# Kernel tuning notes

Measured on AMD Instinct MI355X. Metric: run time of the kernel, lower is better.

Reference implementation:

```python
import jax, jax.numpy as jnp
import numpy as np

D_MODEL = 1024
NUM_HEADS = 16
D_K = D_MODEL // NUM_HEADS


def setup_inputs() -> dict:
    key = jax.random.key(0)
    ks = jax.random.split(key, 7)
    B, S = 4, 2048
    lim = float(np.sqrt(6.0 / (D_MODEL + D_MODEL)))  # xavier uniform
    x = jax.random.normal(ks[0], (B, S, D_MODEL), dtype=jnp.float32)
    w_q = jax.random.uniform(ks[1], (D_MODEL, D_MODEL), jnp.float32, -lim, lim)
    w_k = jax.random.uniform(ks[2], (D_MODEL, D_MODEL), jnp.float32, -lim, lim)
    w_v = jax.random.uniform(ks[3], (D_MODEL, D_MODEL), jnp.float32, -lim, lim)
    w_o = jax.random.uniform(ks[4], (D_MODEL, D_MODEL), jnp.float32, -lim, lim)
    b_o = jnp.zeros((D_MODEL,), jnp.float32)
    ln_g = jnp.ones((D_MODEL,), jnp.float32)
    ln_b = jnp.zeros((D_MODEL,), jnp.float32)
    return {"x": x, "w_q": w_q, "w_k": w_k, "w_v": w_v, "w_o": w_o,
            "b_o": b_o, "ln_g": ln_g, "ln_b": ln_b}


def _layer_norm(y, g, b, eps=1e-5):
    mu = jnp.mean(y, axis=-1, keepdims=True)
    var = jnp.var(y, axis=-1, keepdims=True)
    return (y - mu) * jax.lax.rsqrt(var + eps) * g + b


def reference(x, w_q, w_k, w_v, w_o, b_o, ln_g, ln_b):
    B, S, D = x.shape
    # Linear weights stored torch-style [out, in]: y = x @ W^T
    def proj(w):
        return jnp.einsum('bsd,ed->bse', x, w).reshape(B, S, NUM_HEADS, D_K).transpose(0, 2, 1, 3)
    Q, K, V = proj(w_q), proj(w_k), proj(w_v)  # [B, H, S, d_k]
    scores = jnp.einsum('bhqd,bhkd->bhqk', Q, K) / jnp.sqrt(jnp.float32(D_K))
    attn = jax.nn.softmax(scores, axis=-1)  # dropout identity at eval
    out = jnp.einsum('bhqk,bhkd->bhqd', attn, V)  # [B, H, S, d_k]
    out = out.transpose(0, 2, 1, 3).reshape(B, S, D)
    out = jnp.einsum('bsd,ed->bse', out, w_o) + b_o
    return _layer_norm(x + out, ln_g, ln_b)
```

## Files before the change

### kernel.cpp

```cpp
#include <hip/hip_runtime.h>

typedef __bf16 bf16;
typedef bf16 v8bf __attribute__((ext_vector_type(8)));
typedef bf16 v4bf __attribute__((ext_vector_type(4)));
typedef float v4f __attribute__((ext_vector_type(4)));

#define GAS __attribute__((address_space(1)))
#define LAS __attribute__((address_space(3)))

constexpr int D    = 1024;
constexpr int ROWS = 8192;
constexpr int TILE = 128;

__global__ __launch_bounds__(256) void cast_all(
    const float* __restrict__ x,
    const float* __restrict__ wq, const float* __restrict__ wk,
    const float* __restrict__ wv, const float* __restrict__ wo,
    bf16* __restrict__ xb, bf16* __restrict__ wqb, bf16* __restrict__ wkb,
    bf16* __restrict__ wvb, bf16* __restrict__ wob)
{
    int i = blockIdx.x * 256 + threadIdx.x;
    const float* src; bf16* dst; int off;
    if (i < 2 * 1024 * 1024) { src = x; dst = xb; off = i; }
    else {
        int j = i - 2 * 1024 * 1024;
        int w = j >> 18;
        off = j & ((1 << 18) - 1);
        src = (w == 0) ? wq : (w == 1) ? wk : (w == 2) ? wv : wo;
        dst = (w == 0) ? wqb : (w == 1) ? wkb : (w == 2) ? wvb : wob;
    }
    float4 v = ((const float4*)src)[off];
    v4bf o;
    o[0] = (bf16)v.x; o[1] = (bf16)v.y; o[2] = (bf16)v.z; o[3] = (bf16)v.w;
    ((v4bf*)dst)[off] = o;
}

template<int MODE>
__global__ __launch_bounds__(256) void gemm_bt(
    const bf16* __restrict__ A,
    const bf16* __restrict__ W0, const bf16* __restrict__ W1, const bf16* __restrict__ W2,
    bf16* __restrict__ O0, bf16* __restrict__ O1, bf16* __restrict__ O2,
    float* __restrict__ Of, const float* __restrict__ bias,
    const float* __restrict__ X)
{
    __shared__ bf16 As[2][TILE * 32];
    __shared__ bf16 Bs[2][TILE * 32];

    const int tid  = threadIdx.x;
    const int lane = tid & 63;
    const int wave = tid >> 6;
    const int quad = lane >> 4;
    const int l16  = lane & 15;
    const int wm   = (wave >> 1) * 64;
    const int wn   = (wave & 1) * 64;

    const int z = blockIdx.z;
    const bf16* Bw = (MODE == 0) ? ((z == 0) ? W0 : ((z == 1) ? W1 : W2)) : W0;
    bf16*       Ob = (MODE == 0) ? ((z == 0) ? O0 : ((z == 1) ? O1 : O2)) : O0;

    const long rowA0 = (long)blockIdx.y * TILE;
    const long rowB0 = (long)blockIdx.x * TILE;

    const int stRow = wave * 16 + (lane >> 2);
    const int stCol = (lane & 3) * 8;
    const bf16* gA = A  + (rowA0 + stRow) * D + stCol;
    const bf16* gB = Bw + (rowB0 + stRow) * D + stCol;
    const int ldsOff = wave * 16 * 32;

    const v4f vzero = {0.f, 0.f, 0.f, 0.f};
    v4f acc[4][4];
    #pragma unroll
    for (int i = 0; i < 4; i++)
        #pragma unroll
        for (int j = 0; j < 4; j++) acc[i][j] = vzero;

    for (int k0 = 0; k0 < D; k0 += 64) {
        __syncthreads();
        #pragma unroll
        for (int p = 0; p < 2; ++p)
            #pragma unroll
            for (int i = 0; i < 2; ++i) {
                __builtin_amdgcn_global_load_lds(
                    (const GAS void*)(gA + (long)i * 64 * D + p * 32),
                    (LAS void*)(&As[p][ldsOff + i * 64 * 32]), 16, 0, 0);
                __builtin_amdgcn_global_load_lds(
                    (const GAS void*)(gB + (long)i * 64 * D + p * 32),
                    (LAS void*)(&Bs[p][ldsOff + i * 64 * 32]), 16, 0, 0);
            }
        gA += 64; gB += 64;
        __syncthreads();

        #pragma unroll
        for (int p = 0; p < 2; ++p) {
            v8bf a[4], b[4];
            #pragma unroll
            for (int mi = 0; mi < 4; mi++)
                a[mi] = *(const v8bf*)(&As[p][(wm + mi * 16 + l16) * 32 + quad * 8]);
            #pragma unroll
            for (int ni = 0; ni < 4; ni++)
                b[ni] = *(const v8bf*)(&Bs[p][(wn + ni * 16 + l16) * 32 + quad * 8]);
            #pragma unroll
            for (int mi = 0; mi < 4; mi++)
                #pragma unroll
                for (int ni = 0; ni < 4; ni++)
                    acc[mi][ni] = __builtin_amdgcn_mfma_f32_16x16x32_bf16(a[mi], b[ni], acc[mi][ni], 0, 0, 0);
        }
    }

    const float qscale = 0.125f * 1.44269504f;

    if (MODE == 0 && z == 2) {
        #pragma unroll
        for (int mi = 0; mi < 4; mi++) {
            #pragma unroll
            for (int ni = 0; ni < 4; ni++) {
                const long col = rowB0 + wn + ni * 16 + l16;
                const long h_ = col >> 6, dd = col & 63;
                const long row0 = rowA0 + wm + mi * 16 + quad * 4;
                const long b_ = row0 >> 11, s0 = row0 & 2047;
                v4bf pk;
                #pragma unroll
                for (int r = 0; r < 4; r++) pk[r] = (bf16)acc[mi][ni][r];
                *(v4bf*)(Ob + ((b_ * 16 + h_) * 64 + dd) * 2048 + s0) = pk;
            }
        }
    } else {
        #pragma unroll
        for (int mi = 0; mi < 4; mi++) {
            #pragma unroll
            for (int ni = 0; ni < 4; ni++) {
                const long col = rowB0 + wn + ni * 16 + l16;
                float bv = (MODE == 1) ? bias[col] : 0.f;
                #pragma unroll
                for (int r = 0; r < 4; r++) {
                    const long row = rowA0 + wm + mi * 16 + quad * 4 + r;
                    float v = acc[mi][ni][r];
                    if (MODE == 1) Of[row * D + col] = v + bv + X[row * D + col];
                    else {
                        if (z == 0) v *= qscale;
                        Ob[row * D + col] = (bf16)v;
                    }
                }
            }
        }
    }
}

__global__ __launch_bounds__(256) void attn_kernel(
    const bf16* __restrict__ Q, const bf16* __restrict__ Kg,
    const bf16* __restrict__ VtG, bf16* __restrict__ O)
{
    const int qt = blockIdx.x, h = blockIdx.y, b = blockIdx.z;
    const int tid  = threadIdx.x;
    const int lane = tid & 63;
    const int wave = tid >> 6;
    const int quad = lane >> 4;
    const int l16  = lane & 15;

    __shared__ bf16 Kt[64 * 72];
    __shared__ bf16 Vt[64 * 72];
    __shared__ bf16 Ps[4][32 * 72];

    v8bf qB[2][2];
    #pragma unroll
    for (int qf = 0; qf < 2; qf++) {
        const long qrow = (long)(b * 2048 + qt * 128 + wave * 32 + qf * 16 + l16);
        #pragma unroll
        for (int hh = 0; hh < 2; hh++)
            qB[qf][hh] = *(const v8bf*)(Q + qrow * D + h * 64 + hh * 32 + quad * 8);
    }

    float l_acc[2] = {0.f, 0.f};
    v4f o_acc[2][4];
    const v4f vzero = {0.f, 0.f, 0.f, 0.f};
    #pragma unroll
    for (int qf = 0; qf < 2; qf++)
        #pragma unroll
        for (int nf = 0; nf < 4; nf++) o_acc[qf][nf] = vzero;

    const int sC = (tid & 7) * 8;
    const int iR = tid >> 3;

    const bf16* kLane = Kg  + (long)b * 2048 * D + h * 64 + sC + (long)iR * D;
    const bf16* vLane = VtG + (long)(b * 16 + h) * 64 * 2048 + sC + (long)iR * 2048;
    bf16* ktW = Kt + iR * 72 + sC;
    bf16* vtW = Vt + iR * 72 + sC;

    v8bf kpre[2], vpre[2];
    kpre[0] = *(const v8bf*)(kLane);
    kpre[1] = *(const v8bf*)(kLane + 32 * D);
    vpre[0] = *(const v8bf*)(vLane);
    vpre[1] = *(const v8bf*)(vLane + 32 * 2048);
    kLane += 64 * D;
    vLane += 64;

    for (int kt = 0; kt < 32; ++kt) {
        __syncthreads();
        *(v8bf*)(ktW)            = kpre[0];
        *(v8bf*)(ktW + 32 * 72)  = kpre[1];
        *(v8bf*)(vtW)            = vpre[0];
        *(v8bf*)(vtW + 32 * 72)  = vpre[1];
        __syncthreads();

        if (kt + 1 < 32) {
            kpre[0] = *(const v8bf*)(kLane);
            kpre[1] = *(const v8bf*)(kLane + 32 * D);
            vpre[0] = *(const v8bf*)(vLane);
            vpre[1] = *(const v8bf*)(vLane + 32 * 2048);
            kLane += 64 * D;
            vLane += 64;
        }

        v4f st[4][2];
        #pragma unroll
        for (int kf = 0; kf < 4; kf++) {
            v8bf kA0 = *(const v8bf*)(Kt + (kf * 16 + l16) * 72 + quad * 8);
            v8bf kA1 = *(const v8bf*)(Kt + (kf * 16 + l16) * 72 + 32 + quad * 8);
            #pragma unroll
            for (int qf = 0; qf < 2; qf++) {
                v4f t = vzero;
                t = __builtin_amdgcn_mfma_f32_16x16x32_bf16(kA0, qB[qf][0], t, 0, 0, 0);
                t = __builtin_amdgcn_mfma_f32_16x16x32_bf16(kA1, qB[qf][1], t, 0, 0, 0);
                st[kf][qf] = t;
            }
        }

        #pragma unroll
        for (int qf = 0; qf < 2; qf++)
            #pragma unroll
            for (int kf = 0; kf < 4; kf++) {
                v4bf pk;
                #pragma unroll
                for (int r = 0; r < 4; r++) {
                    float p = __builtin_amdgcn_exp2f(st[kf][qf][r]);
                    l_acc[qf] += p;
                    pk[r] = (bf16)p;
                }
                *(v4bf*)(&Ps[wave][(qf * 16 + l16) * 72 + kf * 16 + quad * 4]) = pk;
            }

        #pragma unroll
        for (int ks = 0; ks < 2; ++ks) {
            v8bf vb[4];
            #pragma unroll
            for (int nf = 0; nf < 4; nf++)
                vb[nf] = *(const v8bf*)(Vt + (nf * 16 + l16) * 72 + ks * 32 + quad * 8);
            #pragma unroll
            for (int qf = 0; qf < 2; qf++) {
                v8bf pa = *(const v8bf*)(&Ps[wave][(qf * 16 + l16) * 72 + ks * 32 + quad * 8]);
                #pragma unroll
                for (int nf = 0; nf < 4; nf++)
                    o_acc[qf][nf] = __builtin_amdgcn_mfma_f32_16x16x32_bf16(pa, vb[nf], o_acc[qf][nf], 0, 0, 0);
            }
        }
    }

    #pragma unroll
    for (int qf = 0; qf < 2; qf++) {
        float l = l_acc[qf];
        l += __shfl_xor(l, 16);
        l += __shfl_xor(l, 32);
        l_acc[qf] = l;
    }

    #pragma unroll
    for (int qf = 0; qf < 2; qf++) {
        float inv[4];
        #pragma unroll
        for (int r = 0; r < 4; r++) {
            const int src = (quad << 4) | (quad * 4 + r);
            inv[r] = 1.f / __shfl(l_acc[qf], src);
        }
        const long orow = (long)(b * 2048 + qt * 128 + wave * 32 + qf * 16 + quad * 4);
        #pragma unroll
        for (int nf = 0; nf < 4; nf++)
            #pragma unroll
            for (int r = 0; r < 4; r++)
                O[(orow + r) * D + h * 64 + nf * 16 + l16] = (bf16)(o_acc[qf][nf][r] * inv[r]);
    }
}

__global__ __launch_bounds__(256) void ln_kernel(
    const float* __restrict__ g, const float* __restrict__ beta,
    float* __restrict__ out)
{
    const int row = blockIdx.x;
    const int t = threadIdx.x;
    const int lane = t & 63, wave = t >> 6;
    const long base = (long)row * D + t * 4;

    float4 yv = *(const float4*)(out + base);
    float y0 = yv.x, y1 = yv.y, y2 = yv.z, y3 = yv.w;
    float s1 = y0 + y1 + y2 + y3;
    float s2 = y0*y0 + y1*y1 + y2*y2 + y3*y3;
    #pragma unroll
    for (int off = 1; off < 64; off <<= 1) {
        s1 += __shfl_xor(s1, off);
        s2 += __shfl_xor(s2, off);
    }
    __shared__ float r1[4], r2[4];
    if (lane == 0) { r1[wave] = s1; r2[wave] = s2; }
    __syncthreads();
    float S1 = r1[0] + r1[1] + r1[2] + r1[3];
    float S2 = r2[0] + r2[1] + r2[2] + r2[3];
    float mu  = S1 * (1.f / 1024.f);
    float var = S2 * (1.f / 1024.f) - mu * mu;
    float rsd = rsqrtf(var + 1e-5f);

    float4 gv = *(const float4*)(g + t * 4);
    float4 bv = *(const float4*)(beta + t * 4);
    float4 o;
    o.x = (y0 - mu) * rsd * gv.x + bv.x;
    o.y = (y1 - mu) * rsd * gv.y + bv.y;
    o.z = (y2 - mu) * rsd * gv.z + bv.z;
    o.w = (y3 - mu) * rsd * gv.w + bv.w;
    *(float4*)(out + base) = o;
}

extern "C" void kernel_launch(void* const* d_in, const int* in_sizes, int n_in,
                              void* d_out, int out_size, void* d_ws, size_t ws_size,
                              hipStream_t stream)
{
    const float* x   = (const float*)d_in[0];
    const float* wq  = (const float*)d_in[1];
    const float* wk  = (const float*)d_in[2];
    const float* wv  = (const float*)d_in[3];
    const float* wo  = (const float*)d_in[4];
    const float* bo  = (const float*)d_in[5];
    const float* lng = (const float*)d_in[6];
    const float* lnb = (const float*)d_in[7];
    float* out = (float*)d_out;

    char* ws = (char*)d_ws;
    bf16* xb  = (bf16*)(ws);
    bf16* wqb = (bf16*)(ws + (size_t)16 * 1024 * 1024);
    bf16* wkb = wqb + 1024 * 1024;
    bf16* wvb = wkb + 1024 * 1024;
    bf16* wob = wvb + 1024 * 1024;
    bf16* Qb  = (bf16*)(ws + (size_t)24 * 1024 * 1024);
    bf16* Kb  = Qb + (size_t)ROWS * D;
    bf16* VtG = Kb + (size_t)ROWS * D;
    bf16* Ab  = VtG + (size_t)ROWS * D;

    cast_all<<<12288, 256, 0, stream>>>(x, wq, wk, wv, wo,
                                        xb, wqb, wkb, wvb, wob);

    dim3 gqkv(D / TILE, ROWS / TILE, 3);
    gemm_bt<0><<<gqkv, 256, 0, stream>>>(xb, wqb, wkb, wvb, Qb, Kb, VtG,
                                         nullptr, nullptr, nullptr);

    attn_kernel<<<dim3(16, 16, 4), 256, 0, stream>>>(Qb, Kb, VtG, Ab);

    dim3 gout(D / TILE, ROWS / TILE, 1);
    gemm_bt<1><<<gout, 256, 0, stream>>>(Ab, wob, nullptr, nullptr,
                                         nullptr, nullptr, nullptr, out, bo, x);

    ln_kernel<<<8192, 256, 0, stream>>>(lng, lnb, out);
}
```

Before: 316.6 us.

## Rewrite attention inner loop with 32x32 MFMA and in-register P transpose

Switches the attention kernel from 16x16x32 MFMA tiles to 32x32x16 tiles. The softmax probabilities are converted to bf16 and rearranged across lanes with permlane32 swaps, so they feed the PV MFMA straight from registers instead of going through a per-wave shared-memory buffer. The K/V shared tiles drop their padding and use an XOR swizzle to avoid bank conflicts. The intent is to cut LDS traffic and synchronisation per tile and raise MFMA efficiency, at the cost of inline asm that depends on the exact lane layout.

```diff
diff --git a/kernel.cpp b/kernel.cpp
--- a/kernel.cpp
+++ b/kernel.cpp
@@ -4,6 +4,9 @@
 typedef bf16 v8bf __attribute__((ext_vector_type(8)));
 typedef bf16 v4bf __attribute__((ext_vector_type(4)));
 typedef float v4f __attribute__((ext_vector_type(4)));
+typedef float v16f __attribute__((ext_vector_type(16)));
+typedef unsigned int u32;
+typedef u32 v4u __attribute__((ext_vector_type(4)));
 
 #define GAS __attribute__((address_space(1)))
 #define LAS __attribute__((address_space(3)))
@@ -154,37 +157,33 @@
     const int tid  = threadIdx.x;
     const int lane = tid & 63;
     const int wave = tid >> 6;
-    const int quad = lane >> 4;
-    const int l16  = lane & 15;
-
-    __shared__ bf16 Kt[64 * 72];
-    __shared__ bf16 Vt[64 * 72];
-    __shared__ bf16 Ps[4][32 * 72];
-
-    v8bf qB[2][2];
-    #pragma unroll
-    for (int qf = 0; qf < 2; qf++) {
-        const long qrow = (long)(b * 2048 + qt * 128 + wave * 32 + qf * 16 + l16);
-        #pragma unroll
-        for (int hh = 0; hh < 2; hh++)
-            qB[qf][hh] = *(const v8bf*)(Q + qrow * D + h * 64 + hh * 32 + quad * 8);
-    }
-
-    float l_acc[2] = {0.f, 0.f};
-    v4f o_acc[2][4];
-    const v4f vzero = {0.f, 0.f, 0.f, 0.f};
-    #pragma unroll
-    for (int qf = 0; qf < 2; qf++)
-        #pragma unroll
-        for (int nf = 0; nf < 4; nf++) o_acc[qf][nf] = vzero;
-
-    const int sC = (tid & 7) * 8;
+    const int l31  = lane & 31;
+    const int hi   = lane >> 5;
+
+    __shared__ bf16 Kt[64 * 64];
+    __shared__ bf16 Vt[64 * 64];
+
+    const long qrow = (long)(b * 2048 + qt * 128 + wave * 32 + l31);
+    v8bf qB[4];
+    #pragma unroll
+    for (int f = 0; f < 4; f++)
+        qB[f] = *(const v8bf*)(Q + qrow * D + h * 64 + f * 16 + hi * 8);
+
+    v16f o_acc[2];
+    #pragma unroll
+    for (int d2 = 0; d2 < 2; d2++)
+        #pragma unroll
+        for (int i = 0; i < 16; i++) o_acc[d2][i] = 0.f;
+    float l_acc = 0.f;
+
     const int iR = tid >> 3;
-
+    const int c8 = tid & 7;
+    const int sC = c8 * 8;
     const bf16* kLane = Kg  + (long)b * 2048 * D + h * 64 + sC + (long)iR * D;
     const bf16* vLane = VtG + (long)(b * 16 + h) * 64 * 2048 + sC + (long)iR * 2048;
-    bf16* ktW = Kt + iR * 72 + sC;
-    bf16* vtW = Vt + iR * 72 + sC;
+    const int wOff = iR * 64 + ((c8 ^ (iR & 7)) * 8);
+    bf16* ktW = Kt + wOff;
+    bf16* vtW = Vt + wOff;
 
     v8bf kpre[2], vpre[2];
     kpre[0] = *(const v8bf*)(kLane);
@@ -197,9 +196,9 @@
     for (int kt = 0; kt < 32; ++kt) {
         __syncthreads();
         *(v8bf*)(ktW)            = kpre[0];
-        *(v8bf*)(ktW + 32 * 72)  = kpre[1];
+        *(v8bf*)(ktW + 32 * 64)  = kpre[1];
         *(v8bf*)(vtW)            = vpre[0];
-        *(v8bf*)(vtW + 32 * 72)  = vpre[1];
+        *(v8bf*)(vtW + 32 * 64)  = vpre[1];
         __syncthreads();
 
         if (kt + 1 < 32) {
@@ -211,72 +210,57 @@
             vLane += 64;
         }
 
-        v4f st[4][2];
-        #pragma unroll
-        for (int kf = 0; kf < 4; kf++) {
-            v8bf kA0 = *(const v8bf*)(Kt + (kf * 16 + l16) * 72 + quad * 8);
-            v8bf kA1 = *(const v8bf*)(Kt + (kf * 16 + l16) * 72 + 32 + quad * 8);
-            #pragma unroll
-            for (int qf = 0; qf < 2; qf++) {
-                v4f t = vzero;
-                t = __builtin_amdgcn_mfma_f32_16x16x32_bf16(kA0, qB[qf][0], t, 0, 0, 0);
-                t = __builtin_amdgcn_mfma_f32_16x16x32_bf16(kA1, qB[qf][1], t, 0, 0, 0);
-                st[kf][qf] = t;
-            }
-        }
-
-        #pragma unroll
-        for (int qf = 0; qf < 2; qf++)
-            #pragma unroll
-            for (int kf = 0; kf < 4; kf++) {
-                v4bf pk;
+        #pragma unroll
+        for (int ko = 0; ko < 2; ko++) {
+            v16f st;
+            #pragma unroll
+            for (int i = 0; i < 16; i++) st[i] = 0.f;
+            const int krow = ko * 32 + l31;
+            const int ksw  = krow & 7;
+            #pragma unroll
+            for (int f = 0; f < 4; f++) {
+                v8bf kA = *(const v8bf*)(Kt + krow * 64 + (((2 * f + hi) ^ ksw) * 8));
+                st = __builtin_amdgcn_mfma_f32_32x32x16_bf16(kA, qB[f], st, 0, 0, 0);
+            }
+
+            float p[16];
+            #pragma unroll
+            for (int r = 0; r < 16; r++) {
+                p[r] = __builtin_amdgcn_exp2f(st[r]);
+                l_acc += p[r];
+            }
+
+            #pragma unroll
+            for (int u = 0; u < 2; u++) {
+                const int s = ko * 2 + u;
+                u32 a0, a1, b0, b1;
+                asm("v_cvt_pk_bf16_f32 %0, %1, %2" : "=v"(a0) : "v"(p[u*8+0]), "v"(p[u*8+1]));
+                asm("v_cvt_pk_bf16_f32 %0, %1, %2" : "=v"(a1) : "v"(p[u*8+2]), "v"(p[u*8+3]));
+                asm("v_cvt_pk_bf16_f32 %0, %1, %2" : "=v"(b0) : "v"(p[u*8+4]), "v"(p[u*8+5]));
+                asm("v_cvt_pk_bf16_f32 %0, %1, %2" : "=v"(b1) : "v"(p[u*8+6]), "v"(p[u*8+7]));
+                asm("v_permlane32_swap_b32 %0, %1" : "+v"(a0), "+v"(b0));
+                asm("v_permlane32_swap_b32 %0, %1" : "+v"(a1), "+v"(b1));
+                v4u w; w[0] = a0; w[1] = a1; w[2] = b0; w[3] = b1;
+                const v8bf pa = __builtin_bit_cast(v8bf, w);
                 #pragma unroll
-                for (int r = 0; r < 4; r++) {
-                    float p = __builtin_amdgcn_exp2f(st[kf][qf][r]);
-                    l_acc[qf] += p;
-                    pk[r] = (bf16)p;
+                for (int d2 = 0; d2 < 2; d2++) {
+                    const int vrow = d2 * 32 + l31;
+                    v8bf vb = *(const v8bf*)(Vt + vrow * 64 + (((2 * s + hi) ^ (vrow & 7)) * 8));
+                    o_acc[d2] = __builtin_amdgcn_mfma_f32_32x32x16_bf16(pa, vb, o_acc[d2], 0, 0, 0);
                 }
-                *(v4bf*)(&Ps[wave][(qf * 16 + l16) * 72 + kf * 16 + quad * 4]) = pk;
-            }
-
-        #pragma unroll
-        for (int ks = 0; ks < 2; ++ks) {
-            v8bf vb[4];
-            #pragma unroll
-            for (int nf = 0; nf < 4; nf++)
-                vb[nf] = *(const v8bf*)(Vt + (nf * 16 + l16) * 72 + ks * 32 + quad * 8);
-            #pragma unroll
-            for (int qf = 0; qf < 2; qf++) {
-                v8bf pa = *(const v8bf*)(&Ps[wave][(qf * 16 + l16) * 72 + ks * 32 + quad * 8]);
-                #pragma unroll
-                for (int nf = 0; nf < 4; nf++)
-                    o_acc[qf][nf] = __builtin_amdgcn_mfma_f32_16x16x32_bf16(pa, vb[nf], o_acc[qf][nf], 0, 0, 0);
-            }
-        }
-    }
-
-    #pragma unroll
-    for (int qf = 0; qf < 2; qf++) {
-        float l = l_acc[qf];
-        l += __shfl_xor(l, 16);
-        l += __shfl_xor(l, 32);
-        l_acc[qf] = l;
-    }
-
-    #pragma unroll
-    for (int qf = 0; qf < 2; qf++) {
-        float inv[4];
-        #pragma unroll
-        for (int r = 0; r < 4; r++) {
-            const int src = (quad << 4) | (quad * 4 + r);
-            inv[r] = 1.f / __shfl(l_acc[qf], src);
-        }
-        const long orow = (long)(b * 2048 + qt * 128 + wave * 32 + qf * 16 + quad * 4);
-        #pragma unroll
-        for (int nf = 0; nf < 4; nf++)
-            #pragma unroll
-            for (int r = 0; r < 4; r++)
-                O[(orow + r) * D + h * 64 + nf * 16 + l16] = (bf16)(o_acc[qf][nf][r] * inv[r]);
+            }
+        }
+    }
+
+    l_acc += __shfl_xor(l_acc, 32);
+
+    const long obase = (long)(b * 2048 + qt * 128 + wave * 32);
+    #pragma unroll
+    for (int r = 0; r < 16; r++) {
+        const int qp = (r & 3) + 8 * (r >> 2) + 4 * hi;
+        const float inv = 1.f / __shfl(l_acc, qp);
+        O[(obase + qp) * D + h * 64 + l31]      = (bf16)(o_acc[0][r] * inv);
+        O[(obase + qp) * D + h * 64 + 32 + l31] = (bf16)(o_acc[1][r] * inv);
     }
 }
 
```

New measurement: 310.9 us. Within noise of the previous version (-1.8%).
